# Kernel optimization log

Measured on AMD Instinct MI355X. Metric: run time of the kernel, lower is better.

The kernel has to match this reference:

```python
import jax, jax.numpy as jnp
import numpy as np

B, S, E = 4, 2048, 1024

def setup_inputs() -> dict:
    key = jax.random.key(0)
    ks = jax.random.split(key, 6)
    values = jax.random.normal(ks[0], (B, S, E), dtype=jnp.float32)
    keys_t = jax.random.normal(ks[1], (B, S, E), dtype=jnp.float32)
    query = jax.random.normal(ks[2], (B, S, E), dtype=jnp.float32)
    mask = jax.random.randint(ks[3], (B, 1, S), 0, 2, dtype=jnp.int32)
    W_out = jax.random.normal(ks[4], (E, E), dtype=jnp.float32) * (1.0 / np.sqrt(E))
    b_out = jax.random.normal(ks[5], (E,), dtype=jnp.float32) * 0.01
    return {"values": values, "keys": keys_t, "query": query, "mask": mask,
            "W_out": W_out, "b_out": b_out}

def reference(values, keys, query, mask, W_out, b_out):
    # scores: [B, S, S] = Q K^T / sqrt(embed_size)  (NOTE: module scales by
    # sqrt(embed_size), not sqrt(head_dim), and never applies q/k/v Linears)
    scale = 1.0 / jnp.sqrt(jnp.asarray(E, dtype=query.dtype))
    scores = jnp.einsum('bqe,bke->bqk', query, keys) * scale
    scores = jnp.where(mask == 0, -jnp.inf, scores)  # masked_fill(mask==0, -inf)
    attn = jax.nn.softmax(scores, axis=-1)
    out = jnp.einsum('bqk,bke->bqe', attn, values)
    # fc_out: torch Linear -> x @ W^T + b
    return out @ W_out.T + b_out
```

## Files before the change

kernel.cpp:

```cpp
#include <hip/hip_runtime.h>

#define BB 4
#define SS 2048
#define EE 1024

typedef _Float16 f16;
typedef _Float16 f16x4 __attribute__((ext_vector_type(4)));
typedef _Float16 f16x8 __attribute__((ext_vector_type(8)));
typedef float f32x4 __attribute__((ext_vector_type(4)));

typedef const __attribute__((address_space(1))) void* gas_ptr;
typedef __attribute__((address_space(3))) void* las_ptr;

__device__ __forceinline__ void gl_lds16(const void* g, void* l) {
  __builtin_amdgcn_global_load_lds((gas_ptr)g, (las_ptr)l, 16, 0, 0);
}

#define BAR() __builtin_amdgcn_s_barrier()
#define PRIO1() __builtin_amdgcn_s_setprio(1)
#define PRIO0() __builtin_amdgcn_s_setprio(0)
#define WAITV8() asm volatile("s_waitcnt vmcnt(8)" ::: "memory")
#define WAITV6() asm volatile("s_waitcnt vmcnt(6)" ::: "memory")
#define WAITV4() asm volatile("s_waitcnt vmcnt(4)" ::: "memory")
#define WAITV0() asm volatile("s_waitcnt vmcnt(0)" ::: "memory")

__global__ __launch_bounds__(256) void prep(const int* __restrict__ mask,
                                            int* __restrict__ pos,
                                            int2* __restrict__ cnt,
                                            f16* __restrict__ Kc,
                                            f16* __restrict__ Vc) {
  const int b = blockIdx.x, t = threadIdx.x;
  const int* mb = mask + b * SS;
  int4 a0 = ((const int4*)mb)[t * 2];
  int4 a1 = ((const int4*)mb)[t * 2 + 1];
  int m[8] = {a0.x, a0.y, a0.z, a0.w, a1.x, a1.y, a1.z, a1.w};
  int tot = 0;
#pragma unroll
  for (int j = 0; j < 8; ++j) tot += m[j];
  __shared__ int sc[256];
  sc[t] = tot;
  __syncthreads();
  for (int off = 1; off < 256; off <<= 1) {
    int v = (t >= off) ? sc[t - off] : 0;
    __syncthreads();
    sc[t] += v;
    __syncthreads();
  }
  const int count = sc[255];
  const int padded = (count + 255) & ~255;
  int run = sc[t] - tot;
#pragma unroll
  for (int j = 0; j < 8; ++j) {
    pos[b * SS + t * 8 + j] = run;
    run += m[j];
  }
  if (t == 0) cnt[b] = make_int2(count, padded);
  const int nz = (padded - count) * 128;
  f16x8 z = {};
  for (int i = t; i < nz; i += 256) {
    int r = count + (i >> 7), cc = i & 127;
    ((f16x8*)(Kc + ((long)b * SS + r) * EE))[cc] = z;
    ((f16x8*)(Vc + ((long)b * SS + r) * EE))[cc] = z;
  }
}

__global__ __launch_bounds__(256) void prep2(const float* __restrict__ Q,
                                             const float* __restrict__ W,
                                             const float* __restrict__ K,
                                             const float* __restrict__ V,
                                             const int* __restrict__ mask,
                                             const int* __restrict__ pos,
                                             const int2* __restrict__ cnt,
                                             f16* __restrict__ Qh,
                                             f16* __restrict__ Wh,
                                             f16* __restrict__ Kc,
                                             f16* __restrict__ Vc,
                                             float* __restrict__ rowsum,
                                             int* __restrict__ items,
                                             int* __restrict__ nit) {
  const int x = blockIdx.x, t = threadIdx.x;
  if (x < 4608) {
    const float* in = (x < 4096) ? Q : W;
    f16* out = (x < 4096) ? Qh : Wh;
    long i = (long)(x < 4096 ? x : x - 4096) * 256 + t;
    float4 v0 = ((const float4*)in)[i * 2];
    float4 v1 = ((const float4*)in)[i * 2 + 1];
    f16x8 o;
    o[0] = (f16)v0.x; o[1] = (f16)v0.y; o[2] = (f16)v0.z; o[3] = (f16)v0.w;
    o[4] = (f16)v1.x; o[5] = (f16)v1.y; o[6] = (f16)v1.z; o[7] = (f16)v1.w;
    ((f16x8*)out)[i] = o;
    return;
  }
  if (x == 4608) {
    float4 z = {0.f, 0.f, 0.f, 0.f};
#pragma unroll
    for (int r = 0; r < 8; ++r) ((float4*)rowsum)[t + r * 256] = z;
    return;
  }
  if (x == 4609) {
    if (t < 8) {
      int nbx[4];
#pragma unroll
      for (int zz = 0; zz < 4; ++zz) nbx[zz] = cnt[zz].y >> 8;
      int mxn = nbx[0];
#pragma unroll
      for (int zz = 1; zz < 4; ++zz) mxn = nbx[zz] > mxn ? nbx[zz] : mxn;
      const int mx = 6 * mxn;
      const int bz = t >> 1, half = t & 1;
      int g = 0;
      for (int q = 0; q < 4; ++q)
        for (int bx = 0; bx < nbx[bz]; ++bx)
          items[(g++ << 3) | t] = bx | ((half * 4 + q) << 8) | (bz << 16);
      for (int q = 0; q < 2; ++q)
        for (int bx = 0; bx < nbx[bz]; ++bx)
          items[(g++ << 3) | t] = bx | ((half * 2 + q) << 8) | (bz << 16) | (1 << 24);
      for (; g < mx; ++g) items[(g << 3) | t] = (3 << 24);
      if (t == 0) nit[0] = mx << 3;
    }
    return;
  }
  const int r = x - 4610, b = r >> 11, s = r & (SS - 1);
  if (!mask[b * SS + s]) return;
  const int p = pos[b * SS + s];
  float4 kv = ((const float4*)(K + ((long)b * SS + s) * EE))[t];
  float4 vv = ((const float4*)(V + ((long)b * SS + s) * EE))[t];
  f16x4 ko, vo;
  ko[0] = (f16)kv.x; ko[1] = (f16)kv.y; ko[2] = (f16)kv.z; ko[3] = (f16)kv.w;
  vo[0] = (f16)vv.x; vo[1] = (f16)vv.y; vo[2] = (f16)vv.z; vo[3] = (f16)vv.w;
  ((f16x4*)(Kc + ((long)b * SS + p) * EE))[t] = ko;
  ((f16x4*)(Vc + ((long)b * SS + p) * EE))[t] = vo;
}

__device__ __forceinline__ void stage64(const f16* g, long K, f16* l, int h, int t) {
  int rr = t >> 3, sp = t & 7;
  int row = h * 64 + rr;
  int sl = sp ^ (rr & 7);
  gl_lds16(g + (long)row * K + (sl << 3), (char*)l + ((row << 6) + (sp << 3)) * 2);
}

__device__ __forceinline__ void read_a(f16x8 (&d)[4][2], const f16* base, int q,
                                       int wm, int l15, int l4) {
#pragma unroll
  for (int mf = 0; mf < 4; ++mf)
#pragma unroll
    for (int kk = 0; kk < 2; ++kk) {
      int row = wm * 128 + (q * 4 + mf) * 16 + l15;
      int sl = kk * 4 + l4;
      d[mf][kk] = *(const f16x8*)(base + row * 64 + ((sl ^ (row & 7)) << 3));
    }
}

__device__ __forceinline__ void read_b2(f16x8 (&d)[2][2], const f16* base, int nh,
                                        int wn, int l15, int l4) {
#pragma unroll
  for (int nf = 0; nf < 2; ++nf)
#pragma unroll
    for (int kk = 0; kk < 2; ++kk) {
      int row = wn * 64 + (nh * 2 + nf) * 16 + l15;
      int sl = kk * 4 + l4;
      d[nf][kk] = *(const f16x8*)(base + row * 64 + ((sl ^ (row & 7)) << 3));
    }
}

__device__ __forceinline__ void read_b1(f16x8 (&d)[2], const f16* base, int f,
                                        int wn, int l15, int l4) {
#pragma unroll
  for (int kk = 0; kk < 2; ++kk) {
    int row = wn * 32 + f * 16 + l15;
    int sl = kk * 4 + l4;
    d[kk] = *(const f16x8*)(base + row * 64 + ((sl ^ (row & 7)) << 3));
  }
}

__device__ __forceinline__ void mfma_q(f32x4 (&acc)[8][4], const f16x8 (&Af)[4][2],
                                       const f16x8 (&Bf)[2][2], int q, int nh) {
#pragma unroll
  for (int mf = 0; mf < 4; ++mf)
#pragma unroll
    for (int nf = 0; nf < 2; ++nf)
#pragma unroll
      for (int kk = 0; kk < 2; ++kk)
        acc[q * 4 + mf][nh * 2 + nf] = __builtin_amdgcn_mfma_f32_16x16x32_f16(
            Af[mf][kk], Bf[nf][kk], acc[q * 4 + mf][nh * 2 + nf], 0, 0, 0);
}

__device__ __forceinline__ void mfma_n(f32x4 (&acc)[8][2], const f16x8 (&Af)[4][2],
                                       const f16x8 (&Bf)[2], int q, int f) {
#pragma unroll
  for (int mf = 0; mf < 4; ++mf)
#pragma unroll
    for (int kk = 0; kk < 2; ++kk)
      acc[q * 4 + mf][f] = __builtin_amdgcn_mfma_f32_16x16x32_f16(
          Af[mf][kk], Bf[kk], acc[q * 4 + mf][f], 0, 0, 0);
}

__device__ __forceinline__ void g256_core(f32x4 (&acc)[8][4], const f16* Ag,
                                          const f16* Bg, long L, int NT,
                                          f16* lds, int tid, int wm, int wn,
                                          int l15, int l4) {
  f16* As0 = lds;
  f16* As1 = lds + 16384;
  f16* Bs0 = lds + 32768;
  f16* Bs1 = lds + 49152;
  f16x8 a[4][2], b[2][2], b2[2][2];
  const int NIT = NT >> 1;

#pragma unroll
  for (int h = 0; h < 4; ++h) stage64(Bg, L, Bs0, h, tid);
#pragma unroll
  for (int h = 0; h < 4; ++h) stage64(Ag, L, As0, h, tid);
#pragma unroll
  for (int h = 0; h < 4; ++h) stage64(Bg + 64, L, Bs1, h, tid);
#pragma unroll
  for (int h = 0; h < 4; ++h) stage64(Ag + 64, L, As1, h, tid);
  WAITV8();
  BAR();

  for (int i = 0; i < NIT; ++i) {
    int t2 = 2 * i + 2, t3 = 2 * i + 3;
    long k2 = (long)((t2 < NT) ? t2 : NT - 1) << 6;
    long k3 = (long)((t3 < NT) ? t3 : NT - 1) << 6;
    read_a(a, As0, 0, wm, l15, l4);
    read_b2(b, Bs0, 0, wn, l15, l4);
    BAR(); PRIO1(); mfma_q(acc, a, b, 0, 0); PRIO0(); BAR();
    read_b2(b2, Bs0, 1, wn, l15, l4);
    BAR(); PRIO1(); mfma_q(acc, a, b2, 0, 1); PRIO0(); BAR();
    read_a(a, As0, 1, wm, l15, l4);
    stage64(Bg + k2, L, Bs0, 0, tid); stage64(Bg + k2, L, Bs0, 1, tid);
    BAR(); PRIO1(); mfma_q(acc, a, b2, 1, 1); PRIO0(); BAR();
    stage64(Bg + k2, L, Bs0, 2, tid); stage64(Bg + k2, L, Bs0, 3, tid);
    BAR(); PRIO1(); mfma_q(acc, a, b, 1, 0); PRIO0();
    WAITV4();
    BAR();
    read_a(a, As1, 0, wm, l15, l4);
    read_b2(b, Bs1, 0, wn, l15, l4);
    stage64(Ag + k2, L, As0, 0, tid); stage64(Ag + k2, L, As0, 1, tid);
    BAR(); PRIO1(); mfma_q(acc, a, b, 0, 0); PRIO0(); BAR();
    read_b2(b2, Bs1, 1, wn, l15, l4);
    stage64(Ag + k2, L, As0, 2, tid); stage64(Ag + k2, L, As0, 3, tid);
    BAR(); PRIO1(); mfma_q(acc, a, b2, 0, 1); PRIO0(); BAR();
    read_a(a, As1, 1, wm, l15, l4);
    stage64(Bg + k3, L, Bs1, 0, tid); stage64(Bg + k3, L, Bs1, 1, tid);
    BAR(); PRIO1(); mfma_q(acc, a, b2, 1, 1); PRIO0(); BAR();
    stage64(Bg + k3, L, Bs1, 2, tid); stage64(Bg + k3, L, Bs1, 3, tid);
    stage64(Ag + k3, L, As1, 0, tid); stage64(Ag + k3, L, As1, 1, tid);
    stage64(Ag + k3, L, As1, 2, tid); stage64(Ag + k3, L, As1, 3, tid);
    BAR(); PRIO1(); mfma_q(acc, a, b, 1, 0); PRIO0();
    WAITV8();
    BAR();
  }
  WAITV0();
}

__device__ __forceinline__ void n128_core(f32x4 (&acc)[8][2], const f16* Ag,
                                          const f16* Bg, long L, int NT,
                                          f16* lds, int tid, int wm, int wn,
                                          int l15, int l4) {
  f16* As0 = lds;
  f16* As1 = lds + 16384;
  f16* Bs0 = lds + 32768;
  f16* Bs1 = lds + 40960;
  f16x8 a[4][2], b[2], b2[2];
  const int NIT = NT >> 1;

  stage64(Bg, L, Bs0, 0, tid); stage64(Bg, L, Bs0, 1, tid);
#pragma unroll
  for (int h = 0; h < 4; ++h) stage64(Ag, L, As0, h, tid);
  stage64(Bg + 64, L, Bs1, 0, tid); stage64(Bg + 64, L, Bs1, 1, tid);
#pragma unroll
  for (int h = 0; h < 4; ++h) stage64(Ag + 64, L, As1, h, tid);
  WAITV6();
  BAR();

  for (int i = 0; i < NIT; ++i) {
    int t2 = 2 * i + 2, t3 = 2 * i + 3;
    long k2 = (long)((t2 < NT) ? t2 : NT - 1) << 6;
    long k3 = (long)((t3 < NT) ? t3 : NT - 1) << 6;
    read_a(a, As0, 0, wm, l15, l4);
    read_b1(b, Bs0, 0, wn, l15, l4);
    BAR(); PRIO1(); mfma_n(acc, a, b, 0, 0); PRIO0(); BAR();
    read_b1(b2, Bs0, 1, wn, l15, l4);
    BAR(); PRIO1(); mfma_n(acc, a, b2, 0, 1); PRIO0(); BAR();
    read_a(a, As0, 1, wm, l15, l4);
    stage64(Bg + k2, L, Bs0, 0, tid); stage64(Bg + k2, L, Bs0, 1, tid);
    BAR(); PRIO1(); mfma_n(acc, a, b2, 1, 1); PRIO0(); BAR();
#pragma unroll
    for (int h = 0; h < 4; ++h) stage64(Ag + k2, L, As0, h, tid);
    BAR(); PRIO1(); mfma_n(acc, a, b, 1, 0); PRIO0();
    WAITV6();
    BAR();
    read_a(a, As1, 0, wm, l15, l4);
    read_b1(b, Bs1, 0, wn, l15, l4);
    BAR(); PRIO1(); mfma_n(acc, a, b, 0, 0); PRIO0(); BAR();
    read_b1(b2, Bs1, 1, wn, l15, l4);
    BAR(); PRIO1(); mfma_n(acc, a, b2, 0, 1); PRIO0(); BAR();
    read_a(a, As1, 1, wm, l15, l4);
    stage64(Bg + k3, L, Bs1, 0, tid); stage64(Bg + k3, L, Bs1, 1, tid);
    BAR(); PRIO1(); mfma_n(acc, a, b2, 1, 1); PRIO0(); BAR();
#pragma unroll
    for (int h = 0; h < 4; ++h) stage64(Ag + k3, L, As1, h, tid);
    BAR(); PRIO1(); mfma_n(acc, a, b, 1, 0); PRIO0();
    WAITV6();
    BAR();
  }
  WAITV0();
}

__global__ __launch_bounds__(512, 1) void uber(const f16* __restrict__ Qh,
                                               const f16* __restrict__ Kc,
                                               const f16* __restrict__ Vc,
                                               const f16* __restrict__ Wh,
                                               f16* __restrict__ P,
                                               f16* __restrict__ VWt,
                                               float* __restrict__ rowsum,
                                               const int2* __restrict__ cnt,
                                               const int* __restrict__ items,
                                               const int* __restrict__ nit) {
  extern __shared__ f16 lds[];
  const int tid = threadIdx.x;
  const int lane = tid & 63, wv = tid >> 6;
  const int wm = wv >> 2, wn = wv & 3;
  const int l15 = lane & 15, l4 = lane >> 4;
  const int n = nit[0];

  for (int idx = blockIdx.x; idx < n; idx += 256) {
    const int it = items[idx];
    const int kind = (it >> 24) & 3;
    if (kind == 3) continue;
    const int bx = it & 255, by = (it >> 8) & 255, bz = (it >> 16) & 255;
    const long m0 = (long)by * 256;
    const long n0 = (long)bx * 256;
    const f16* Ag = kind ? (Wh + m0 * EE) : (Qh + (long)bz * SS * EE + m0 * EE);
    const f16* Bg = (kind ? Vc : Kc) + (long)bz * SS * EE + n0 * EE;

    f32x4 acc[8][4] = {};
    g256_core(acc, Ag, Bg, EE, EE >> 6, lds, tid, wm, wn, l15, l4);

    const long crow = m0 + wm * 128 + l4 * 4;
    const long ccol = n0 + wn * 64 + l15;
    if (kind == 0) {
      const int count = cnt[bz].x;
      f16* Co = P + (long)bz * SS * SS;
      float* rs = rowsum + (bz << 11);
      const float scale = 1.0f / 32.0f;
      int mv[4];
#pragma unroll
      for (int nf = 0; nf < 4; ++nf) mv[nf] = (ccol + nf * 16) < count;
#pragma unroll
      for (int mf = 0; mf < 8; ++mf)
#pragma unroll
        for (int jj = 0; jj < 4; ++jj) {
          float rp = 0.f;
#pragma unroll
          for (int nf = 0; nf < 4; ++nf) {
            float p = mv[nf] ? __expf(acc[mf][nf][jj] * scale) : 0.f;
            Co[(crow + mf * 16 + jj) * SS + ccol + nf * 16] = (f16)p;
            rp += p;
          }
          rp += __shfl_xor(rp, 1); rp += __shfl_xor(rp, 2);
          rp += __shfl_xor(rp, 4); rp += __shfl_xor(rp, 8);
          if (l15 == 0) atomicAdd(&rs[crow + mf * 16 + jj], rp);
        }
    } else {
      f16* Co = VWt + (long)bz * EE * SS;
#pragma unroll
      for (int mf = 0; mf < 8; ++mf)
#pragma unroll
        for (int nf = 0; nf < 4; ++nf)
#pragma unroll
          for (int jj = 0; jj < 4; ++jj)
            Co[(crow + mf * 16 + jj) * SS + ccol + nf * 16] = (f16)acc[mf][nf][jj];
    }
  }
}

__global__ __launch_bounds__(512, 1) void pv128(const f16* __restrict__ P,
                                                const f16* __restrict__ VWt,
                                                float* __restrict__ out,
                                                const float* __restrict__ bias,
                                                const float* __restrict__ rowsum,
                                                const int2* __restrict__ cnt) {
  extern __shared__ f16 lds[];
  const int d = blockIdx.x;
  const int x = d & 7, r = d >> 3;
  const int bz = x >> 1;
  const int by = (x & 1) * 4 + (r & 3);
  const int bx = r >> 2;
  int2 cc = cnt[bz];
  const int padded = cc.y;
  if (padded <= 0) return;
  const long m0 = (long)by * 256;
  const long n0 = (long)bx * 128;
  const int tid = threadIdx.x;
  const int lane = tid & 63, wv = tid >> 6;
  const int wm = wv >> 2, wn = wv & 3;
  const int l15 = lane & 15, l4 = lane >> 4;
  const f16* Ag = P + (long)bz * SS * SS + m0 * SS;
  const f16* Bg = VWt + (long)bz * EE * SS + n0 * SS;

  f32x4 acc[8][2] = {};
  n128_core(acc, Ag, Bg, SS, padded >> 6, lds, tid, wm, wn, l15, l4);

  const long crow = m0 + wm * 128 + l4 * 4;
  const long ccol = n0 + wn * 32 + l15;
  float* Co = out + (long)bz * SS * EE;
  const float* rs = rowsum + (bz << 11);
  float bv[2];
#pragma unroll
  for (int nf = 0; nf < 2; ++nf) bv[nf] = bias[ccol + nf * 16];
#pragma unroll
  for (int mf = 0; mf < 8; ++mf)
#pragma unroll
    for (int jj = 0; jj < 4; ++jj) {
      float inv = 1.f / rs[crow + mf * 16 + jj];
#pragma unroll
      for (int nf = 0; nf < 2; ++nf)
        Co[(crow + mf * 16 + jj) * EE + ccol + nf * 16] =
            acc[mf][nf][jj] * inv + bv[nf];
    }
}

extern "C" void kernel_launch(void* const* d_in, const int* in_sizes, int n_in,
                              void* d_out, int out_size, void* d_ws, size_t ws_size,
                              hipStream_t stream) {
  const float* V = (const float*)d_in[0];
  const float* Kin = (const float*)d_in[1];
  const float* Q = (const float*)d_in[2];
  const int* mask = (const int*)d_in[3];
  const float* W = (const float*)d_in[4];
  const float* bias = (const float*)d_in[5];
  float* out = (float*)d_out;

  const long NE = (long)BB * SS * EE;
  f16* Qh = (f16*)d_ws;
  f16* Kc = Qh + NE;
  f16* Vc = Kc + NE;
  f16* Wh = Vc + NE;
  f16* VWt = Wh + (long)EE * EE;
  f16* P = VWt + NE;
  float* rowsum = (float*)(P + (long)BB * SS * SS);
  int* pos = (int*)(rowsum + (long)BB * SS);
  int2* cnt = (int2*)(pos + (long)BB * SS);
  int* items = (int*)(cnt + BB);
  int* nit = items + 1024;

  const size_t LDS_Q = 131072, LDS_N = 98304;
  hipFuncSetAttribute((const void*)uber, hipFuncAttributeMaxDynamicSharedMemorySize, LDS_Q);
  hipFuncSetAttribute((const void*)pv128, hipFuncAttributeMaxDynamicSharedMemorySize, LDS_N);

  prep<<<BB, 256, 0, stream>>>(mask, pos, cnt, Kc, Vc);
  prep2<<<4610 + BB * SS, 256, 0, stream>>>(Q, W, Kin, V, mask, pos, cnt,
                                            Qh, Wh, Kc, Vc, rowsum, items, nit);
  uber<<<256, 512, LDS_Q, stream>>>(Qh, Kc, Vc, Wh, P, VWt, rowsum, cnt, items, nit);
  pv128<<<256, 512, LDS_N, stream>>>(P, VWt, out, bias, rowsum, cnt);
}
```

Baseline: 97.59 us.

## Pad compacted keys to 128 and remap prep block order for locality

Compacted K/V rows are now padded to a multiple of 128 instead of 256. This shrinks the zero-fill work and any padding rows the attention kernel processes, and the tile count is rounded up to compensate. The Q conversion and K/V compaction blocks get a permuted block-index mapping, likely to interleave batches and halves so they line up with the downstream work-item order or spread memory traffic across channels. The risk is that the last partial 256-key tile now holds up to 128 zero rows, so the attention kernel must handle padded rows correctly.

```diff
diff --git a/kernel.cpp b/kernel.cpp
--- a/kernel.cpp
+++ b/kernel.cpp
@@ -47,7 +47,7 @@
     __syncthreads();
   }
   const int count = sc[255];
-  const int padded = (count + 255) & ~255;
+  const int padded = (count + 127) & ~127;
   int run = sc[t] - tot;
 #pragma unroll
   for (int j = 0; j < 8; ++j) {
@@ -79,16 +79,27 @@
                                              int* __restrict__ items,
                                              int* __restrict__ nit) {
   const int x = blockIdx.x, t = threadIdx.x;
-  if (x < 4608) {
-    const float* in = (x < 4096) ? Q : W;
-    f16* out = (x < 4096) ? Qh : Wh;
-    long i = (long)(x < 4096 ? x : x - 4096) * 256 + t;
-    float4 v0 = ((const float4*)in)[i * 2];
-    float4 v1 = ((const float4*)in)[i * 2 + 1];
+  if (x < 4096) {
+    const int e = x & 7, k = x >> 3;
+    const int bz = e >> 1, half = e & 1, q = k >> 7, off = k & 127;
+    const long logical = (long)((bz * 8 + half * 4 + q) << 7) + off;
+    long i = logical * 256 + t;
+    float4 v0 = ((const float4*)Q)[i * 2];
+    float4 v1 = ((const float4*)Q)[i * 2 + 1];
     f16x8 o;
     o[0] = (f16)v0.x; o[1] = (f16)v0.y; o[2] = (f16)v0.z; o[3] = (f16)v0.w;
     o[4] = (f16)v1.x; o[5] = (f16)v1.y; o[6] = (f16)v1.z; o[7] = (f16)v1.w;
-    ((f16x8*)out)[i] = o;
+    ((f16x8*)Qh)[i] = o;
+    return;
+  }
+  if (x < 4608) {
+    long i = (long)(x - 4096) * 256 + t;
+    float4 v0 = ((const float4*)W)[i * 2];
+    float4 v1 = ((const float4*)W)[i * 2 + 1];
+    f16x8 o;
+    o[0] = (f16)v0.x; o[1] = (f16)v0.y; o[2] = (f16)v0.z; o[3] = (f16)v0.w;
+    o[4] = (f16)v1.x; o[5] = (f16)v1.y; o[6] = (f16)v1.z; o[7] = (f16)v1.w;
+    ((f16x8*)Wh)[i] = o;
     return;
   }
   if (x == 4608) {
@@ -101,7 +112,7 @@
     if (t < 8) {
       int nbx[4];
 #pragma unroll
-      for (int zz = 0; zz < 4; ++zz) nbx[zz] = cnt[zz].y >> 8;
+      for (int zz = 0; zz < 4; ++zz) nbx[zz] = (cnt[zz].y + 255) >> 8;
       int mxn = nbx[0];
 #pragma unroll
       for (int zz = 1; zz < 4; ++zz) mxn = nbx[zz] > mxn ? nbx[zz] : mxn;
@@ -119,7 +130,10 @@
     }
     return;
   }
-  const int r = x - 4610, b = r >> 11, s = r & (SS - 1);
+  const int g = x - 4610;
+  const int e = (g + 2) & 7;
+  const int b = e >> 1;
+  const int s = ((g >> 3) << 1) | (e & 1);
   if (!mask[b * SS + s]) return;
   const int p = pos[b * SS + s];
   float4 kv = ((const float4*)(K + ((long)b * SS + s) * EE))[t];
```

Result: faster. 91.70 us, median of 2 (-6.0%).
